# Kernel tuning notes

Hardware: AMD Instinct MI355X
Metric: run time of the kernel (lower is better)

## Reference

```python
import jax, jax.numpy as jnp
import numpy as np

NEG_SLOPE = 0.2  # PyG GATConv default leaky_relu slope


def gat_conv(x, src, dst, n, W, a_src, a_dst, b):
    """Single-head PyG GATConv (self-loops already included in src/dst)."""
    h = x @ W                                  # [N, F]
    alpha_s = h @ a_src                        # [N]
    alpha_d = h @ a_dst                        # [N]
    e = jax.nn.leaky_relu(alpha_s[src] + alpha_d[dst], NEG_SLOPE)  # [E]
    m = jax.ops.segment_max(e, dst, num_segments=n)
    e = jnp.exp(e - m[dst])
    s = jax.ops.segment_sum(e, dst, num_segments=n)
    alpha = e / s[dst]                         # softmax over incoming edges
    out = jax.ops.segment_sum(alpha[:, None] * h[src], dst, num_segments=n)
    return out + b


def setup_inputs() -> dict:
    key = jax.random.key(0)
    ks = jax.random.split(key, 12)
    N, E = 8192, 262144
    IN, H, OUT, K = 512, 128, 64, 16
    x = jax.random.normal(ks[0], (N, IN), dtype=jnp.float32)
    edge_index = jax.random.randint(ks[1], (2, E), 0, N, dtype=jnp.int32)
    def glorot(k, shape):
        lim = np.sqrt(6.0 / (shape[0] + shape[-1]))
        return jax.random.uniform(k, shape, jnp.float32, -lim, lim)
    return {
        "x": x,
        "edge_index": edge_index,
        "W1": glorot(ks[2], (IN, H)),
        "a_src1": glorot(ks[3], (H,)),
        "a_dst1": glorot(ks[4], (H,)),
        "b1": jnp.zeros((H,), jnp.float32),
        "W2": glorot(ks[5], (H, OUT)),
        "a_src2": glorot(ks[6], (OUT,)),
        "a_dst2": glorot(ks[7], (OUT,)),
        "b2": jnp.zeros((OUT,), jnp.float32),
        "centers": glorot(ks[8], (K, OUT)),
    }


def reference(x, edge_index, W1, a_src1, a_dst1, b1, W2, a_src2, a_dst2, b2, centers):
    n = x.shape[0]
    # add self loops (PyG GATConv default add_self_loops=True)
    loop = jnp.arange(n, dtype=edge_index.dtype)
    src = jnp.concatenate([edge_index[0], loop])
    dst = jnp.concatenate([edge_index[1], loop])
    h = jax.nn.elu(gat_conv(x, src, dst, n, W1, a_src1, a_dst1, b1))
    z = gat_conv(h, src, dst, n, W2, a_src2, a_dst2, b2)       # [N, D]
    A_pred = jax.nn.sigmoid(z @ z.T)                            # [N, N]
    # Student-t soft assignment: [N, K]
    d2 = jnp.sum((z[:, None, :] - centers[None, :, :]) ** 2, axis=2)
    q = 1.0 / (1.0 + d2)
    q = q / jnp.sum(q, axis=1, keepdims=True)
    return (z, A_pred, q)
```

## Files before the change

### kernel.cpp

```cpp
#include <hip/hip_runtime.h>
#include <hip/hip_bf16.h>

typedef __bf16 v8bf __attribute__((ext_vector_type(8)));
typedef float  v4f  __attribute__((ext_vector_type(4)));

__device__ __forceinline__ float lrelu02(float x){ return x > 0.f ? x : 0.2f*x; }

__device__ __forceinline__ unsigned short f2bf_rn(float f){
  unsigned int u = __float_as_uint(f);
  u += 0x7fffu + ((u >> 16) & 1u);
  return (unsigned short)(u >> 16);
}
__device__ __forceinline__ float bf2f(unsigned short h){
  return __uint_as_float(((unsigned int)h) << 16);
}

__global__ void zero_int_kernel(int* p, int n){
  int i = blockIdx.x*blockDim.x + threadIdx.x;
  if (i < n) p[i] = 0;
}

__global__ void hist_kernel(const int* __restrict__ dst, int* counts, int E){
  int i = blockIdx.x*blockDim.x + threadIdx.x;
  if (i < E) atomicAdd(&counts[dst[i]], 1);
}

__global__ void scan_kernel(const int* __restrict__ counts, int* ptr, int* cursor, int n){
  __shared__ int sd[1024];
  int t = threadIdx.x;
  int base = t*8;
  int v[8]; int s = 0;
  #pragma unroll
  for (int i = 0; i < 8; ++i){ int x = (base+i < n) ? counts[base+i] : 0; v[i] = x; s += x; }
  sd[t] = s; __syncthreads();
  for (int off = 1; off < 1024; off <<= 1){
    int x = (t >= off) ? sd[t-off] : 0;
    __syncthreads();
    sd[t] += x;
    __syncthreads();
  }
  int run = sd[t] - s;
  #pragma unroll
  for (int i = 0; i < 8; ++i){
    if (base+i < n){ ptr[base+i] = run; cursor[base+i] = run; run += v[i]; }
  }
  if (t == 1023) ptr[n] = run;
}

__global__ void scatter_kernel(const int* __restrict__ src, const int* __restrict__ dst,
                               int* cursor, int* csr_src, int E){
  int i = blockIdx.x*blockDim.x + threadIdx.x;
  if (i < E){
    int p = atomicAdd(&cursor[dst[i]], 1);
    csr_src[p] = src[i];
  }
}

template<int BM,int BN,int BK,int TM,int TN>
__global__ __launch_bounds__(256) void gemm_tiled(const float* __restrict__ A,
    const float* __restrict__ B, float* __restrict__ C, int M, int N, int K){
  __shared__ float As[BK][BM+1];
  __shared__ float Bs[BK][BN+1];
  const int tid = threadIdx.x;
  const int tx = tid % (BN/TN);
  const int ty = tid / (BN/TN);
  const int brow = blockIdx.y*BM;
  const int bcol = blockIdx.x*BN;
  float acc[TM][TN] = {};
  for (int k0 = 0; k0 < K; k0 += BK){
    for (int i = tid; i < BM*BK; i += 256){
      int m = i / BK, kk = i % BK;
      As[kk][m] = A[(size_t)(brow+m)*K + k0 + kk];
    }
    for (int i = tid; i < BK*BN; i += 256){
      int kk = i / BN, nn = i % BN;
      Bs[kk][nn] = B[(size_t)(k0+kk)*N + bcol + nn];
    }
    __syncthreads();
    #pragma unroll
    for (int kk = 0; kk < BK; ++kk){
      float a[TM], b[TN];
      #pragma unroll
      for (int m = 0; m < TM; ++m) a[m] = As[kk][ty*TM+m];
      #pragma unroll
      for (int n = 0; n < TN; ++n) b[n] = Bs[kk][tx*TN+n];
      #pragma unroll
      for (int m = 0; m < TM; ++m)
        #pragma unroll
        for (int n = 0; n < TN; ++n) acc[m][n] += a[m]*b[n];
    }
    __syncthreads();
  }
  #pragma unroll
  for (int m = 0; m < TM; ++m)
    #pragma unroll
    for (int n = 0; n < TN; ++n)
      C[(size_t)(brow+ty*TM+m)*N + bcol+tx*TN+n] = acc[m][n];
}

__global__ void alpha_kernel(const float* __restrict__ h, const float* __restrict__ avs,
                             const float* __restrict__ avd, float* as_out, float* ad_out,
                             int n, int F){
  int wid = (blockIdx.x*blockDim.x + threadIdx.x) >> 6;
  int lane = threadIdx.x & 63;
  if (wid >= n) return;
  float ps = 0.f, pd = 0.f;
  for (int c = lane; c < F; c += 64){
    float hv = h[(size_t)wid*F + c];
    ps += hv * avs[c];
    pd += hv * avd[c];
  }
  for (int o = 32; o; o >>= 1){ ps += __shfl_xor(ps, o); pd += __shfl_xor(pd, o); }
  if (lane == 0){ as_out[wid] = ps; ad_out[wid] = pd; }
}

template<int FCH, bool ELU>
__global__ void gat_agg(const float* __restrict__ h, const float* __restrict__ as,
                        const float* __restrict__ ad, const int* __restrict__ ptr,
                        const int* __restrict__ csr_src, const float* __restrict__ bias,
                        float* __restrict__ out, int n){
  const int F = FCH*64;
  int wid = (blockIdx.x*blockDim.x + threadIdx.x) >> 6;
  int lane = threadIdx.x & 63;
  if (wid >= n) return;
  const int v = wid;
  const int beg = ptr[v], end = ptr[v+1];
  const float adv = ad[v];
  const float asv = as[v];
  float m = lrelu02(asv + adv);
  for (int j = beg + lane; j < end; j += 64)
    m = fmaxf(m, lrelu02(as[csr_src[j]] + adv));
  for (int o = 32; o; o >>= 1) m = fmaxf(m, __shfl_xor(m, o));
  float acc0 = 0.f, acc1 = 0.f, ssum = 0.f;
  float wself = __expf(lrelu02(asv + adv) - m);
  if (lane == 0) ssum += wself;
  acc0 += wself * h[(size_t)v*F + lane];
  if (FCH == 2) acc1 += wself * h[(size_t)v*F + 64 + lane];
  for (int b0 = beg; b0 < end; b0 += 64){
    int j = b0 + lane;
    float wv = 0.f; int sv = 0;
    if (j < end){
      sv = csr_src[j];
      wv = __expf(lrelu02(as[sv] + adv) - m);
      ssum += wv;
    }
    int cnt = min(64, end - b0);
    for (int t = 0; t < cnt; ++t){
      float wt = __shfl(wv, t);
      int   st = __shfl(sv, t);
      acc0 += wt * h[(size_t)st*F + lane];
      if (FCH == 2) acc1 += wt * h[(size_t)st*F + 64 + lane];
    }
  }
  for (int o = 32; o; o >>= 1) ssum += __shfl_xor(ssum, o);
  float inv = 1.f / ssum;
  float r0 = acc0*inv + bias[lane];
  if (ELU) r0 = r0 > 0.f ? r0 : __expf(r0) - 1.f;
  out[(size_t)v*F + lane] = r0;
  if (FCH == 2){
    float r1 = acc1*inv + bias[64 + lane];
    if (ELU) r1 = r1 > 0.f ? r1 : __expf(r1) - 1.f;
    out[(size_t)v*F + 64 + lane] = r1;
  }
}

__global__ void split_kernel(const float* __restrict__ z, unsigned short* hi,
                             unsigned short* lo, int n){
  int i = blockIdx.x*blockDim.x + threadIdx.x;
  if (i >= n) return;
  float f = z[i];
  unsigned short h = f2bf_rn(f);
  float rem = f - bf2f(h);
  hi[i] = h;
  lo[i] = f2bf_rn(rem);
}

__device__ __forceinline__ v8bf ldz(const unsigned short* z, int node, int k){
  return *reinterpret_cast<const v8bf*>(z + ((size_t)node << 6) + k);
}

__global__ __launch_bounds__(256) void apred_kernel(const unsigned short* __restrict__ zhi,
    const unsigned short* __restrict__ zlo, float* __restrict__ out, int N){
  const int lane = threadIdx.x & 63;
  const int wave = threadIdx.x >> 6;
  const int i0 = blockIdx.y*64 + wave*16;
  const int j0 = blockIdx.x*64;
  const int r = lane & 15, q = lane >> 4;
  const int arow = i0 + r;
  v8bf ahi0 = ldz(zhi, arow,      q*8);
  v8bf ahi1 = ldz(zhi, arow, 32 + q*8);
  v8bf alo0 = ldz(zlo, arow,      q*8);
  v8bf alo1 = ldz(zlo, arow, 32 + q*8);
  #pragma unroll
  for (int c = 0; c < 4; ++c){
    int brow = j0 + c*16 + r;
    v8bf bhi0 = ldz(zhi, brow,      q*8);
    v8bf bhi1 = ldz(zhi, brow, 32 + q*8);
    v8bf blo0 = ldz(zlo, brow,      q*8);
    v8bf blo1 = ldz(zlo, brow, 32 + q*8);
    v4f acc = {0.f,0.f,0.f,0.f};
    acc = __builtin_amdgcn_mfma_f32_16x16x32_bf16(ahi0, bhi0, acc, 0,0,0);
    acc = __builtin_amdgcn_mfma_f32_16x16x32_bf16(ahi1, bhi1, acc, 0,0,0);
    acc = __builtin_amdgcn_mfma_f32_16x16x32_bf16(ahi0, blo0, acc, 0,0,0);
    acc = __builtin_amdgcn_mfma_f32_16x16x32_bf16(ahi1, blo1, acc, 0,0,0);
    acc = __builtin_amdgcn_mfma_f32_16x16x32_bf16(alo0, bhi0, acc, 0,0,0);
    acc = __builtin_amdgcn_mfma_f32_16x16x32_bf16(alo1, bhi1, acc, 0,0,0);
    float* op = out + (size_t)(i0 + q*4)*N + j0 + c*16 + r;
    #pragma unroll
    for (int t = 0; t < 4; ++t){
      float sg = 1.f / (1.f + __expf(-acc[t]));
      op[(size_t)t*N] = sg;
    }
  }
}

__global__ void q_kernel(const float* __restrict__ z, const float* __restrict__ centers,
                         float* __restrict__ qout, int n, int K){
  int wid = (blockIdx.x*blockDim.x + threadIdx.x) >> 6;
  int lane = threadIdx.x & 63;
  if (wid >= n) return;
  float zv = z[(size_t)wid*64 + lane];
  float myq = 0.f, tot = 0.f;
  for (int k = 0; k < K; ++k){
    float d = zv - centers[k*64 + lane];
    float d2 = d*d;
    for (int o = 32; o; o >>= 1) d2 += __shfl_xor(d2, o);
    float qq = 1.f / (1.f + d2);
    if (lane == k) myq = qq;
    tot += qq;
  }
  if (lane < K) qout[(size_t)wid*K + lane] = myq / tot;
}

extern "C" void kernel_launch(void* const* d_in, const int* in_sizes, int n_in,
                              void* d_out, int out_size, void* d_ws, size_t ws_size,
                              hipStream_t stream) {
  const float* x      = (const float*)d_in[0];
  const int*   ei     = (const int*)  d_in[1];
  const float* W1     = (const float*)d_in[2];
  const float* a_src1 = (const float*)d_in[3];
  const float* a_dst1 = (const float*)d_in[4];
  const float* b1     = (const float*)d_in[5];
  const float* W2     = (const float*)d_in[6];
  const float* a_src2 = (const float*)d_in[7];
  const float* a_dst2 = (const float*)d_in[8];
  const float* b2     = (const float*)d_in[9];
  const float* cent   = (const float*)d_in[10];

  const int H   = in_sizes[3];
  const int OUTF= in_sizes[7];
  const int INF = in_sizes[2] / H;
  const int N   = in_sizes[0] / INF;
  const int E   = in_sizes[1] / 2;
  const int K   = in_sizes[10] / OUTF;

  const int* e_src = ei;
  const int* e_dst = ei + E;

  char* wsp = (char*)d_ws;
  auto alloc = [&](size_t b)->void*{ void* p = (void*)wsp; wsp += (b + 255) & ~(size_t)255; return p; };
  int* counts   = (int*)alloc((size_t)N*4);
  int* ptr      = (int*)alloc((size_t)(N+1)*4);
  int* cursor   = (int*)alloc((size_t)N*4);
  int* csr_src  = (int*)alloc((size_t)E*4);
  float* as1    = (float*)alloc((size_t)N*4);
  float* ad1    = (float*)alloc((size_t)N*4);
  float* as2    = (float*)alloc((size_t)N*4);
  float* ad2    = (float*)alloc((size_t)N*4);
  unsigned short* zhi = (unsigned short*)alloc((size_t)N*OUTF*2);
  unsigned short* zlo = (unsigned short*)alloc((size_t)N*OUTF*2);

  float* out_f  = (float*)d_out;
  float* z_out  = out_f;
  float* ap_out = out_f + (size_t)N*OUTF;
  float* q_out  = ap_out + (size_t)N*N;
  float* h1  = ap_out;
  float* h2  = h1 + (size_t)N*H;
  float* h2w = h2 + (size_t)N*H;

  const int wavesPerGrid = (N*64 + 255)/256;

  zero_int_kernel<<<(N+255)/256, 256, 0, stream>>>(counts, N);
  gemm_tiled<64,64,16,4,4><<<dim3(H/64, N/64), 256, 0, stream>>>(x, W1, h1, N, H, INF);
  alpha_kernel<<<wavesPerGrid, 256, 0, stream>>>(h1, a_src1, a_dst1, as1, ad1, N, H);
  hist_kernel<<<(E+255)/256, 256, 0, stream>>>(e_dst, counts, E);
  scan_kernel<<<1, 1024, 0, stream>>>(counts, ptr, cursor, N);
  scatter_kernel<<<(E+255)/256, 256, 0, stream>>>(e_src, e_dst, cursor, csr_src, E);
  gat_agg<2,true><<<wavesPerGrid, 256, 0, stream>>>(h1, as1, ad1, ptr, csr_src, b1, h2, N);
  gemm_tiled<64,64,16,4,4><<<dim3(OUTF/64, N/64), 256, 0, stream>>>(h2, W2, h2w, N, OUTF, H);
  alpha_kernel<<<wavesPerGrid, 256, 0, stream>>>(h2w, a_src2, a_dst2, as2, ad2, N, OUTF);
  gat_agg<1,false><<<wavesPerGrid, 256, 0, stream>>>(h2w, as2, ad2, ptr, csr_src, b2, z_out, N);
  split_kernel<<<(N*OUTF+255)/256, 256, 0, stream>>>(z_out, zhi, zlo, N*OUTF);
  q_kernel<<<wavesPerGrid, 256, 0, stream>>>(z_out, cent, q_out, N, K);
  apred_kernel<<<dim3(N/64, N/64), 256, 0, stream>>>(zhi, zlo, ap_out, N);
}
```

Measured before the change: 627.8 us.

## Use split-bf16 MFMA for first GEMM, fuse layer-2 epilogue, stage A_pred stores

Replaces the FP32 tiled first-layer GEMM with a split-bf16 (hi/lo) MFMA kernel fed by a new conversion pass over x and a transposed W1. Folds the z split and the Student-t q computation into the second aggregation kernel, which removes two launches and a re-read of z. The A_pred kernel now stages sigmoid results in shared memory and writes 16-byte vector rows, giving coalesced stores to the large N×N output. The new conversion kernel adds an extra read and write of x, and three bf16 products approximate the FP32 matmul.

Result: faster. 565.1 us (-10.0%).

```diff
diff --git a/kernel.cpp b/kernel.cpp
--- a/kernel.cpp
+++ b/kernel.cpp
@@ -54,6 +54,57 @@
     int p = atomicAdd(&cursor[dst[i]], 1);
     csr_src[p] = src[i];
   }
+}
+
+__global__ void convert_kernel(const float* __restrict__ x, const float* __restrict__ W1,
+    unsigned short* xh, unsigned short* xl, unsigned short* wth, unsigned short* wtl,
+    int nx, int nw){
+  int i = blockIdx.x*blockDim.x + threadIdx.x;
+  if (i < nx){
+    float f = x[i];
+    unsigned short h = f2bf_rn(f);
+    xh[i] = h;
+    xl[i] = f2bf_rn(f - bf2f(h));
+  } else if (i < nx + nw){
+    int e = i - nx;
+    int k = e >> 7, n = e & 127;
+    float f = W1[e];
+    unsigned short h = f2bf_rn(f);
+    wth[n*512 + k] = h;
+    wtl[n*512 + k] = f2bf_rn(f - bf2f(h));
+  }
+}
+
+__global__ __launch_bounds__(128) void gemm1_mfma(const unsigned short* __restrict__ xh,
+    const unsigned short* __restrict__ xl, const unsigned short* __restrict__ wth,
+    const unsigned short* __restrict__ wtl, float* __restrict__ h1){
+  const int lane = threadIdx.x & 63;
+  const int wave = threadIdx.x >> 6;
+  const int i0 = blockIdx.x*32 + wave*16;
+  const int r = lane & 15, q = lane >> 4;
+  const unsigned short* xrh = xh + (size_t)(i0 + r)*512;
+  const unsigned short* xrl = xl + (size_t)(i0 + r)*512;
+  v4f acc[8];
+  #pragma unroll
+  for (int c = 0; c < 8; ++c) acc[c] = (v4f){0.f,0.f,0.f,0.f};
+  for (int kt = 0; kt < 16; ++kt){
+    int k = kt*32 + q*8;
+    v8bf ah = *reinterpret_cast<const v8bf*>(xrh + k);
+    v8bf al = *reinterpret_cast<const v8bf*>(xrl + k);
+    #pragma unroll
+    for (int ct = 0; ct < 8; ++ct){
+      v8bf bh = *reinterpret_cast<const v8bf*>(wth + (size_t)(ct*16 + r)*512 + k);
+      v8bf bl = *reinterpret_cast<const v8bf*>(wtl + (size_t)(ct*16 + r)*512 + k);
+      acc[ct] = __builtin_amdgcn_mfma_f32_16x16x32_bf16(ah, bh, acc[ct], 0,0,0);
+      acc[ct] = __builtin_amdgcn_mfma_f32_16x16x32_bf16(al, bh, acc[ct], 0,0,0);
+      acc[ct] = __builtin_amdgcn_mfma_f32_16x16x32_bf16(ah, bl, acc[ct], 0,0,0);
+    }
+  }
+  #pragma unroll
+  for (int ct = 0; ct < 8; ++ct)
+    #pragma unroll
+    for (int t = 0; t < 4; ++t)
+      h1[(size_t)(i0 + q*4 + t)*128 + ct*16 + r] = acc[ct][t];
 }
 
 template<int BM,int BN,int BK,int TM,int TN>
@@ -114,12 +165,11 @@
   if (lane == 0){ as_out[wid] = ps; ad_out[wid] = pd; }
 }
 
-template<int FCH, bool ELU>
-__global__ void gat_agg(const float* __restrict__ h, const float* __restrict__ as,
-                        const float* __restrict__ ad, const int* __restrict__ ptr,
-                        const int* __restrict__ csr_src, const float* __restrict__ bias,
-                        float* __restrict__ out, int n){
-  const int F = FCH*64;
+__global__ void gat_agg1(const float* __restrict__ h, const float* __restrict__ as,
+                         const float* __restrict__ ad, const int* __restrict__ ptr,
+                         const int* __restrict__ csr_src, const float* __restrict__ bias,
+                         float* __restrict__ out, int n){
+  const int F = 128;
   int wid = (blockIdx.x*blockDim.x + threadIdx.x) >> 6;
   int lane = threadIdx.x & 63;
   if (wid >= n) return;
@@ -135,7 +185,7 @@
   float wself = __expf(lrelu02(asv + adv) - m);
   if (lane == 0) ssum += wself;
   acc0 += wself * h[(size_t)v*F + lane];
-  if (FCH == 2) acc1 += wself * h[(size_t)v*F + 64 + lane];
+  acc1 += wself * h[(size_t)v*F + 64 + lane];
   for (int b0 = beg; b0 < end; b0 += 64){
     int j = b0 + lane;
     float wv = 0.f; int sv = 0;
@@ -149,30 +199,73 @@
       float wt = __shfl(wv, t);
       int   st = __shfl(sv, t);
       acc0 += wt * h[(size_t)st*F + lane];
-      if (FCH == 2) acc1 += wt * h[(size_t)st*F + 64 + lane];
+      acc1 += wt * h[(size_t)st*F + 64 + lane];
     }
   }
   for (int o = 32; o; o >>= 1) ssum += __shfl_xor(ssum, o);
   float inv = 1.f / ssum;
   float r0 = acc0*inv + bias[lane];
-  if (ELU) r0 = r0 > 0.f ? r0 : __expf(r0) - 1.f;
+  r0 = r0 > 0.f ? r0 : __expf(r0) - 1.f;
   out[(size_t)v*F + lane] = r0;
-  if (FCH == 2){
-    float r1 = acc1*inv + bias[64 + lane];
-    if (ELU) r1 = r1 > 0.f ? r1 : __expf(r1) - 1.f;
-    out[(size_t)v*F + 64 + lane] = r1;
-  }
-}
-
-__global__ void split_kernel(const float* __restrict__ z, unsigned short* hi,
-                             unsigned short* lo, int n){
-  int i = blockIdx.x*blockDim.x + threadIdx.x;
-  if (i >= n) return;
-  float f = z[i];
-  unsigned short h = f2bf_rn(f);
-  float rem = f - bf2f(h);
-  hi[i] = h;
-  lo[i] = f2bf_rn(rem);
+  float r1 = acc1*inv + bias[64 + lane];
+  r1 = r1 > 0.f ? r1 : __expf(r1) - 1.f;
+  out[(size_t)v*F + 64 + lane] = r1;
+}
+
+__global__ void gat_agg2_fused(const float* __restrict__ h, const float* __restrict__ as,
+                               const float* __restrict__ ad, const int* __restrict__ ptr,
+                               const int* __restrict__ csr_src, const float* __restrict__ bias,
+                               const float* __restrict__ centers,
+                               float* __restrict__ z_out, unsigned short* __restrict__ zhi,
+                               unsigned short* __restrict__ zlo, float* __restrict__ qout,
+                               int n, int K){
+  const int F = 64;
+  int wid = (blockIdx.x*blockDim.x + threadIdx.x) >> 6;
+  int lane = threadIdx.x & 63;
+  if (wid >= n) return;
+  const int v = wid;
+  const int beg = ptr[v], end = ptr[v+1];
+  const float adv = ad[v];
+  const float asv = as[v];
+  float m = lrelu02(asv + adv);
+  for (int j = beg + lane; j < end; j += 64)
+    m = fmaxf(m, lrelu02(as[csr_src[j]] + adv));
+  for (int o = 32; o; o >>= 1) m = fmaxf(m, __shfl_xor(m, o));
+  float acc0 = 0.f, ssum = 0.f;
+  float wself = __expf(lrelu02(asv + adv) - m);
+  if (lane == 0) ssum += wself;
+  acc0 += wself * h[(size_t)v*F + lane];
+  for (int b0 = beg; b0 < end; b0 += 64){
+    int j = b0 + lane;
+    float wv = 0.f; int sv = 0;
+    if (j < end){
+      sv = csr_src[j];
+      wv = __expf(lrelu02(as[sv] + adv) - m);
+      ssum += wv;
+    }
+    int cnt = min(64, end - b0);
+    for (int t = 0; t < cnt; ++t){
+      float wt = __shfl(wv, t);
+      int   st = __shfl(sv, t);
+      acc0 += wt * h[(size_t)st*F + lane];
+    }
+  }
+  for (int o = 32; o; o >>= 1) ssum += __shfl_xor(ssum, o);
+  float r0 = acc0 / ssum + bias[lane];
+  z_out[(size_t)v*F + lane] = r0;
+  unsigned short hh = f2bf_rn(r0);
+  zhi[(size_t)v*F + lane] = hh;
+  zlo[(size_t)v*F + lane] = f2bf_rn(r0 - bf2f(hh));
+  float myq = 0.f, tot = 0.f;
+  for (int k = 0; k < K; ++k){
+    float d = r0 - centers[k*F + lane];
+    float d2 = d*d;
+    for (int o = 32; o; o >>= 1) d2 += __shfl_xor(d2, o);
+    float qq = 1.f / (1.f + d2);
+    if (lane == k) myq = qq;
+    tot += qq;
+  }
+  if (lane < K) qout[(size_t)v*K + lane] = myq / tot;
 }
 
 __device__ __forceinline__ v8bf ldz(const unsigned short* z, int node, int k){
@@ -181,6 +274,7 @@
 
 __global__ __launch_bounds__(256) void apred_kernel(const unsigned short* __restrict__ zhi,
     const unsigned short* __restrict__ zlo, float* __restrict__ out, int N){
+  __shared__ float tile[4][16][68];
   const int lane = threadIdx.x & 63;
   const int wave = threadIdx.x >> 6;
   const int i0 = blockIdx.y*64 + wave*16;
@@ -205,31 +299,19 @@
     acc = __builtin_amdgcn_mfma_f32_16x16x32_bf16(ahi1, blo1, acc, 0,0,0);
     acc = __builtin_amdgcn_mfma_f32_16x16x32_bf16(alo0, bhi0, acc, 0,0,0);
     acc = __builtin_amdgcn_mfma_f32_16x16x32_bf16(alo1, bhi1, acc, 0,0,0);
-    float* op = out + (size_t)(i0 + q*4)*N + j0 + c*16 + r;
     #pragma unroll
     for (int t = 0; t < 4; ++t){
-      float sg = 1.f / (1.f + __expf(-acc[t]));
-      op[(size_t)t*N] = sg;
-    }
-  }
-}
-
-__global__ void q_kernel(const float* __restrict__ z, const float* __restrict__ centers,
-                         float* __restrict__ qout, int n, int K){
-  int wid = (blockIdx.x*blockDim.x + threadIdx.x) >> 6;
-  int lane = threadIdx.x & 63;
-  if (wid >= n) return;
-  float zv = z[(size_t)wid*64 + lane];
-  float myq = 0.f, tot = 0.f;
-  for (int k = 0; k < K; ++k){
-    float d = zv - centers[k*64 + lane];
-    float d2 = d*d;
-    for (int o = 32; o; o >>= 1) d2 += __shfl_xor(d2, o);
-    float qq = 1.f / (1.f + d2);
-    if (lane == k) myq = qq;
-    tot += qq;
-  }
-  if (lane < K) qout[(size_t)wid*K + lane] = myq / tot;
+      float e = __expf(-acc[t]);
+      tile[wave][q*4 + t][c*16 + r] = __builtin_amdgcn_rcpf(1.f + e);
+    }
+  }
+  #pragma unroll
+  for (int t = 0; t < 4; ++t){
+    int row = t*4 + (lane >> 4);
+    int col = (lane & 15)*4;
+    v4f vv = *reinterpret_cast<v4f*>(&tile[wave][row][col]);
+    *reinterpret_cast<v4f*>(out + (size_t)(i0 + row)*N + j0 + col) = vv;
+  }
 }
 
 extern "C" void kernel_launch(void* const* d_in, const int* in_sizes, int n_in,
@@ -269,6 +351,10 @@
   float* ad2    = (float*)alloc((size_t)N*4);
   unsigned short* zhi = (unsigned short*)alloc((size_t)N*OUTF*2);
   unsigned short* zlo = (unsigned short*)alloc((size_t)N*OUTF*2);
+  unsigned short* xh  = (unsigned short*)alloc((size_t)N*INF*2);
+  unsigned short* xl  = (unsigned short*)alloc((size_t)N*INF*2);
+  unsigned short* wth = (unsigned short*)alloc((size_t)INF*H*2);
+  unsigned short* wtl = (unsigned short*)alloc((size_t)INF*H*2);
 
   float* out_f  = (float*)d_out;
   float* z_out  = out_f;
@@ -279,18 +365,19 @@
   float* h2w = h2 + (size_t)N*H;
 
   const int wavesPerGrid = (N*64 + 255)/256;
+  const int nx = N*INF, nw = INF*H;
 
   zero_int_kernel<<<(N+255)/256, 256, 0, stream>>>(counts, N);
-  gemm_tiled<64,64,16,4,4><<<dim3(H/64, N/64), 256, 0, stream>>>(x, W1, h1, N, H, INF);
-  alpha_kernel<<<wavesPerGrid, 256, 0, stream>>>(h1, a_src1, a_dst1, as1, ad1, N, H);
   hist_kernel<<<(E+255)/256, 256, 0, stream>>>(e_dst, counts, E);
   scan_kernel<<<1, 1024, 0, stream>>>(counts, ptr, cursor, N);
   scatter_kernel<<<(E+255)/256, 256, 0, stream>>>(e_src, e_dst, cursor, csr_src, E);
-  gat_agg<2,true><<<wavesPerGrid, 256, 0, stream>>>(h1, as1, ad1, ptr, csr_src, b1, h2, N);
+  convert_kernel<<<(nx+nw+255)/256, 256, 0, stream>>>(x, W1, xh, xl, wth, wtl, nx, nw);
+  gemm1_mfma<<<N/32, 128, 0, stream>>>(xh, xl, wth, wtl, h1);
+  alpha_kernel<<<wavesPerGrid, 256, 0, stream>>>(h1, a_src1, a_dst1, as1, ad1, N, H);
+  gat_agg1<<<wavesPerGrid, 256, 0, stream>>>(h1, as1, ad1, ptr, csr_src, b1, h2, N);
   gemm_tiled<64,64,16,4,4><<<dim3(OUTF/64, N/64), 256, 0, stream>>>(h2, W2, h2w, N, OUTF, H);
   alpha_kernel<<<wavesPerGrid, 256, 0, stream>>>(h2w, a_src2, a_dst2, as2, ad2, N, OUTF);
-  gat_agg<1,false><<<wavesPerGrid, 256, 0, stream>>>(h2w, as2, ad2, ptr, csr_src, b2, z_out, N);
-  split_kernel<<<(N*OUTF+255)/256, 256, 0, stream>>>(z_out, zhi, zlo, N*OUTF);
-  q_kernel<<<wavesPerGrid, 256, 0, stream>>>(z_out, cent, q_out, N, K);
+  gat_agg2_fused<<<wavesPerGrid, 256, 0, stream>>>(h2w, as2, ad2, ptr, csr_src, b2, cent,
+                                                   z_out, zhi, zlo, q_out, N, K);
   apred_kernel<<<dim3(N/64, N/64), 256, 0, stream>>>(zhi, zlo, ap_out, N);
 }
```
